# Optimization experiments

Measured on AMD Instinct MI355X. Metric: run time of the kernel, lower is better.

Reference implementation:

```python
import jax, jax.numpy as jnp
import numpy as np

N_NODES = 100000
N_EDGES = 6400000
IN_NODE = 6
IN_EDGE = 1
HID = 10
OUT = 2


def setup_inputs() -> dict:
    key = jax.random.key(0)
    ks = jax.random.split(key, 8)
    x = jax.random.normal(ks[0], (N_NODES, IN_NODE), dtype=jnp.float32)
    edge_index = jax.random.randint(ks[1], (2, N_EDGES), 0, N_NODES, dtype=jnp.int64)
    edge_attr = jax.random.normal(ks[2], (N_EDGES, IN_EDGE), dtype=jnp.float32)
    edge_attr_T = jax.random.normal(ks[3], (N_EDGES, IN_EDGE), dtype=jnp.float32)
    in_dim = 2 * IN_NODE + IN_EDGE  # 13
    W1 = jax.random.normal(ks[4], (in_dim, HID), dtype=jnp.float32) / np.sqrt(in_dim)
    b1 = jnp.zeros((HID,), dtype=jnp.float32)
    W2 = jax.random.normal(ks[5], (HID, OUT), dtype=jnp.float32) / np.sqrt(HID)
    b2 = jnp.zeros((OUT,), dtype=jnp.float32)
    return {"x": x, "edge_index": edge_index, "edge_attr": edge_attr,
            "edge_attr_T": edge_attr_T, "W1": W1, "b1": b1, "W2": W2, "b2": b2}


def _mlp(feat, W1, b1, W2, b2):
    h = jax.nn.relu(feat @ W1 + b1)
    return h @ W2 + b2


def reference(x, edge_index, edge_attr, edge_attr_T, W1, b1, W2, b2):
    src = edge_index[0]
    tgt = edge_index[1]
    x_src = x[src]  # [E, 6]
    x_tgt = x[tgt]  # [E, 6]
    feat_fwd = jnp.concatenate([x_src, x_tgt, edge_attr], axis=-1)      # [E, 13]
    feat_rev = jnp.concatenate([x_tgt, x_src, edge_attr_T], axis=-1)    # [E, 13]
    out = _mlp(feat_fwd, W1, b1, W2, b2) + _mlp(feat_rev, W1, b1, W2, b2)
    out = out * 0.5
    out = jax.nn.softmax(out, axis=1)
    return out[:, -1:]  # [E, 1]
```

## Files before the change

### kernel.cpp

```cpp
#include <hip/hip_runtime.h>
#include <hip/hip_fp16.h>


__global__ void prep(const float* __restrict__ W1, const float* __restrict__ b1,
                     const float* __restrict__ W2, const float* __restrict__ b2,
                     const float* __restrict__ x, float* __restrict__ ws, int N) {
    int t = blockIdx.x * 256 + threadIdx.x;
    if (t < N) {
        const float2* xr = (const float2*)x;
        float2 a0 = xr[3 * t], a1 = xr[3 * t + 1], a2 = xr[3 * t + 2];
        union { __half2 h[4]; float4 f; } pk;
        pk.h[0] = __floats2half2_rn(a0.x, a0.y);
        pk.h[1] = __floats2half2_rn(a1.x, a1.y);
        pk.h[2] = __floats2half2_rn(a2.x, a2.y);
        pk.h[3] = __floats2half2_rn(0.0f, 0.0f);
        ((float4*)((char*)ws + 4096))[t] = pk.f;
    }
    if (blockIdx.x == 0) {
        int u = threadIdx.x;
        if (u < 60) {
            int i = u / 10, j = u % 10;
            float a = W1[i * 10 + j];
            float c = W1[(i + 6) * 10 + j];
            ws[u]      = 0.5f * (a + c);
            ws[60 + u] = 0.5f * (a - c);
        }
        if (u < 10) {
            ws[120 + u] = W1[120 + u];
            ws[130 + u] = b1[u];
            ws[140 + u] = 0.5f * (W2[u * 2 + 1] - W2[u * 2]);
        }
        if (u == 0) ws[150] = b2[1] - b2[0];
    }
}

__launch_bounds__(256, 8)
__global__ void edge_mlp(const float4* __restrict__ xp, const int* __restrict__ ei,
                         const float* __restrict__ ea, const float* __restrict__ eaT,
                         const float* __restrict__ wg, float* __restrict__ out, int E) {
    int e = blockIdx.x * 256 + threadIdx.x;
    if (e >= E) return;

    int   si   = __builtin_nontemporal_load(ei + e);
    int   ti   = __builtin_nontemporal_load(ei + E + e);
    float fea  = __builtin_nontemporal_load(ea + e);
    float feaT = __builtin_nontemporal_load(eaT + e);

    float4 rs = xp[si];
    float4 rt = xp[ti];
    const __half2* hs = (const __half2*)&rs;
    const __half2* ht = (const __half2*)&rt;

    float sv[6], dv[6];
#pragma unroll
    for (int k = 0; k < 3; ++k) {
        float2 fs = __half22float2(hs[k]);
        float2 ft = __half22float2(ht[k]);
        sv[2 * k]     = fs.x + ft.x;  dv[2 * k]     = fs.x - ft.x;
        sv[2 * k + 1] = fs.y + ft.y;  dv[2 * k + 1] = fs.y - ft.y;
    }

    float cacc[10], macc[10];
#pragma unroll
    for (int j = 0; j < 10; ++j) { cacc[j] = wg[130 + j]; macc[j] = 0.0f; }
#pragma unroll
    for (int i = 0; i < 6; ++i) {
#pragma unroll
        for (int j = 0; j < 10; ++j) {
            cacc[j] = fmaf(sv[i], wg[i * 10 + j],      cacc[j]);
            macc[j] = fmaf(dv[i], wg[60 + i * 10 + j], macc[j]);
        }
    }

    float z = wg[150];
#pragma unroll
    for (int j = 0; j < 10; ++j) {
        float af = fmaf(fea,  wg[120 + j], cacc[j] + macc[j]);
        float ar = fmaf(feaT, wg[120 + j], cacc[j] - macc[j]);
        float h  = fmaxf(af, 0.0f) + fmaxf(ar, 0.0f);
        z = fmaf(h, wg[140 + j], z);
    }

    float r = 1.0f / (1.0f + __expf(-z));
    __builtin_nontemporal_store(r, out + e);
}

extern "C" void kernel_launch(void* const* d_in, const int* in_sizes, int n_in,
                              void* d_out, int out_size, void* d_ws, size_t ws_size,
                              hipStream_t stream) {
    const float* x   = (const float*)d_in[0];
    const int*   ei  = (const int*)d_in[1];
    const float* ea  = (const float*)d_in[2];
    const float* eaT = (const float*)d_in[3];
    const float* W1  = (const float*)d_in[4];
    const float* b1  = (const float*)d_in[5];
    const float* W2  = (const float*)d_in[6];
    const float* b2  = (const float*)d_in[7];
    float* out = (float*)d_out;
    float* ws  = (float*)d_ws;
    int E = in_sizes[2];
    int N = in_sizes[0] / 6;

    int pblocks = (N + 255) / 256;
    prep<<<pblocks, 256, 0, stream>>>(W1, b1, W2, b2, x, ws, N);

    const float4* xp = (const float4*)((char*)d_ws + 4096);
    int blocks = (E + 255) / 256;
    edge_mlp<<<blocks, 256, 0, stream>>>(xp, ei, ea, eaT, ws, out, E);
}
```

Baseline: 195.4 us.

## Use packed fp16 dot products and process two edges per thread

```diff
diff --git a/kernel.cpp b/kernel.cpp
--- a/kernel.cpp
+++ b/kernel.cpp
@@ -2,9 +2,16 @@
 #include <hip/hip_fp16.h>
 
 
+typedef _Float16 half2_t __attribute__((ext_vector_type(2)));
+typedef _Float16 half8_t __attribute__((ext_vector_type(8)));
+typedef float    float2_v __attribute__((ext_vector_type(2)));
+typedef int      int2_v   __attribute__((ext_vector_type(2)));
+
+union h2u { __half2 h; unsigned u; half2_t v; };
+
 __global__ void prep(const float* __restrict__ W1, const float* __restrict__ b1,
                      const float* __restrict__ W2, const float* __restrict__ b2,
-                     const float* __restrict__ x, float* __restrict__ ws, int N) {
+                     const float* __restrict__ x, float* __restrict__ wsf, int N) {
     int t = blockIdx.x * 256 + threadIdx.x;
     if (t < N) {
         const float2* xr = (const float2*)x;
@@ -14,75 +21,114 @@
         pk.h[1] = __floats2half2_rn(a1.x, a1.y);
         pk.h[2] = __floats2half2_rn(a2.x, a2.y);
         pk.h[3] = __floats2half2_rn(0.0f, 0.0f);
-        ((float4*)((char*)ws + 4096))[t] = pk.f;
+        ((float4*)((char*)wsf + 4096))[t] = pk.f;
     }
     if (blockIdx.x == 0) {
+        unsigned* wsu = (unsigned*)wsf;
         int u = threadIdx.x;
-        if (u < 60) {
-            int i = u / 10, j = u % 10;
-            float a = W1[i * 10 + j];
-            float c = W1[(i + 6) * 10 + j];
-            ws[u]      = 0.5f * (a + c);
-            ws[60 + u] = 0.5f * (a - c);
+        if (u < 10) wsf[u] = b1[u];
+        if (u == 0) wsf[10] = b2[1] - b2[0];
+        if (u < 30) {
+            int k = u / 10, j = u % 10;
+            float a0 = W1[(2 * k) * 10 + j],     c0 = W1[(2 * k + 6) * 10 + j];
+            float a1 = W1[(2 * k + 1) * 10 + j], c1 = W1[(2 * k + 7) * 10 + j];
+            h2u p, m;
+            p.h = __floats2half2_rn(0.5f * (a0 + c0), 0.5f * (a1 + c1));
+            m.h = __floats2half2_rn(0.5f * (a0 - c0), 0.5f * (a1 - c1));
+            wsu[16 + u] = p.u;
+            wsu[48 + u] = m.u;
         }
-        if (u < 10) {
-            ws[120 + u] = W1[120 + u];
-            ws[130 + u] = b1[u];
-            ws[140 + u] = 0.5f * (W2[u * 2 + 1] - W2[u * 2]);
+        if (u < 5) {
+            h2u a, b;
+            a.h = __floats2half2_rn(W1[120 + 2 * u], W1[120 + 2 * u + 1]);
+            b.h = __floats2half2_rn(0.5f * (W2[(2 * u) * 2 + 1] - W2[(2 * u) * 2]),
+                                    0.5f * (W2[(2 * u + 1) * 2 + 1] - W2[(2 * u + 1) * 2]));
+            wsu[80 + u] = a.u;
+            wsu[88 + u] = b.u;
         }
-        if (u == 0) ws[150] = b2[1] - b2[0];
     }
 }
 
-__launch_bounds__(256, 8)
-__global__ void edge_mlp(const float4* __restrict__ xp, const int* __restrict__ ei,
-                         const float* __restrict__ ea, const float* __restrict__ eaT,
-                         const float* __restrict__ wg, float* __restrict__ out, int E) {
-    int e = blockIdx.x * 256 + threadIdx.x;
-    if (e >= E) return;
+static __device__ __forceinline__ float fdot2(half2_t a, half2_t b, float c) {
+#if __has_builtin(__builtin_amdgcn_fdot2)
+    return __builtin_amdgcn_fdot2(a, b, c, false);
+#else
+    return fmaf((float)a[0], (float)b[0], fmaf((float)a[1], (float)b[1], c));
+#endif
+}
 
-    int   si   = __builtin_nontemporal_load(ei + e);
-    int   ti   = __builtin_nontemporal_load(ei + E + e);
-    float fea  = __builtin_nontemporal_load(ea + e);
-    float feaT = __builtin_nontemporal_load(eaT + e);
+static __device__ __forceinline__ half2_t h2bc(const unsigned* wsu, int idx) {
+    h2u t; t.u = wsu[idx]; return t.v;
+}
 
-    float4 rs = xp[si];
-    float4 rt = xp[ti];
-    const __half2* hs = (const __half2*)&rs;
-    const __half2* ht = (const __half2*)&rt;
-
-    float sv[6], dv[6];
-#pragma unroll
-    for (int k = 0; k < 3; ++k) {
-        float2 fs = __half22float2(hs[k]);
-        float2 ft = __half22float2(ht[k]);
-        sv[2 * k]     = fs.x + ft.x;  dv[2 * k]     = fs.x - ft.x;
-        sv[2 * k + 1] = fs.y + ft.y;  dv[2 * k + 1] = fs.y - ft.y;
-    }
+static __device__ __forceinline__ float edge_one(half8_t rs, half8_t rt,
+                                                 float fea, float feaT,
+                                                 const float* __restrict__ wsf,
+                                                 const unsigned* __restrict__ wsu) {
+    half8_t sv8 = rs + rt;
+    half8_t dv8 = rs - rt;
+    half2_t sv[3] = { __builtin_shufflevector(sv8, sv8, 0, 1),
+                      __builtin_shufflevector(sv8, sv8, 2, 3),
+                      __builtin_shufflevector(sv8, sv8, 4, 5) };
+    half2_t dv[3] = { __builtin_shufflevector(dv8, dv8, 0, 1),
+                      __builtin_shufflevector(dv8, dv8, 2, 3),
+                      __builtin_shufflevector(dv8, dv8, 4, 5) };
 
     float cacc[10], macc[10];
 #pragma unroll
-    for (int j = 0; j < 10; ++j) { cacc[j] = wg[130 + j]; macc[j] = 0.0f; }
+    for (int j = 0; j < 10; ++j) { cacc[j] = wsf[j]; macc[j] = 0.0f; }
 #pragma unroll
-    for (int i = 0; i < 6; ++i) {
+    for (int k = 0; k < 3; ++k) {
 #pragma unroll
         for (int j = 0; j < 10; ++j) {
-            cacc[j] = fmaf(sv[i], wg[i * 10 + j],      cacc[j]);
-            macc[j] = fmaf(dv[i], wg[60 + i * 10 + j], macc[j]);
+            cacc[j] = fdot2(sv[k], h2bc(wsu, 16 + k * 10 + j), cacc[j]);
+            macc[j] = fdot2(dv[k], h2bc(wsu, 48 + k * 10 + j), macc[j]);
         }
     }
 
-    float z = wg[150];
+    _Float16 feah  = (_Float16)fea,  feaTh = (_Float16)feaT;
+    half2_t fea2  = { feah,  feah  };
+    half2_t feaT2 = { feaTh, feaTh };
+    half2_t zero2 = { (_Float16)0.0f, (_Float16)0.0f };
+
+    float z = wsf[10];
 #pragma unroll
-    for (int j = 0; j < 10; ++j) {
-        float af = fmaf(fea,  wg[120 + j], cacc[j] + macc[j]);
-        float ar = fmaf(feaT, wg[120 + j], cacc[j] - macc[j]);
-        float h  = fmaxf(af, 0.0f) + fmaxf(ar, 0.0f);
-        z = fmaf(h, wg[140 + j], z);
+    for (int jp = 0; jp < 5; ++jp) {
+        half2_t c2 = { (_Float16)cacc[2 * jp], (_Float16)cacc[2 * jp + 1] };
+        half2_t m2 = { (_Float16)macc[2 * jp], (_Float16)macc[2 * jp + 1] };
+        half2_t w12 = h2bc(wsu, 80 + jp);
+        half2_t af2 = __builtin_elementwise_fma(fea2,  w12, c2 + m2);
+        half2_t ar2 = __builtin_elementwise_fma(feaT2, w12, c2 - m2);
+        half2_t h2  = __builtin_elementwise_max(af2, zero2) +
+                      __builtin_elementwise_max(ar2, zero2);
+        z = fdot2(h2, h2bc(wsu, 88 + jp), z);
     }
+    return 1.0f / (1.0f + __expf(-z));
+}
 
-    float r = 1.0f / (1.0f + __expf(-z));
-    __builtin_nontemporal_store(r, out + e);
+__launch_bounds__(256, 8)
+__global__ void edge_mlp(const half8_t* __restrict__ xp, const int* __restrict__ ei,
+                         const float* __restrict__ ea, const float* __restrict__ eaT,
+                         const float* __restrict__ wsf, float* __restrict__ out, int E) {
+    const unsigned* wsu = (const unsigned*)wsf;
+    int g = blockIdx.x * 256 + threadIdx.x;
+    int e0 = 2 * g;
+    if (e0 + 1 < E) {
+        int2_v   s2 = __builtin_nontemporal_load((const int2_v*)(ei + e0));
+        int2_v   t2 = __builtin_nontemporal_load((const int2_v*)(ei + E + e0));
+        float2_v fa = __builtin_nontemporal_load((const float2_v*)(ea + e0));
+        float2_v fT = __builtin_nontemporal_load((const float2_v*)(eaT + e0));
+        half8_t rs0 = xp[s2[0]], rt0 = xp[t2[0]];
+        half8_t rs1 = xp[s2[1]], rt1 = xp[t2[1]];
+        float2_v r;
+        r[0] = edge_one(rs0, rt0, fa[0], fT[0], wsf, wsu);
+        r[1] = edge_one(rs1, rt1, fa[1], fT[1], wsf, wsu);
+        __builtin_nontemporal_store(r, (float2_v*)(out + e0));
+    } else if (e0 < E) {
+        int si = ei[e0], ti = ei[E + e0];
+        float r = edge_one(xp[si], xp[ti], ea[e0], eaT[e0], wsf, wsu);
+        out[e0] = r;
+    }
 }
 
 extern "C" void kernel_launch(void* const* d_in, const int* in_sizes, int n_in,
@@ -104,7 +150,8 @@
     int pblocks = (N + 255) / 256;
     prep<<<pblocks, 256, 0, stream>>>(W1, b1, W2, b2, x, ws, N);
 
-    const float4* xp = (const float4*)((char*)d_ws + 4096);
-    int blocks = (E + 255) / 256;
+    const half8_t* xp = (const half8_t*)((char*)d_ws + 4096);
+    int nthreads = (E + 1) / 2;
+    int blocks = (nthreads + 255) / 256;
     edge_mlp<<<blocks, 256, 0, stream>>>(xp, ei, ea, eaT, ws, out, E);
 }
```

New measurement: 197.8 us. About the same (+1.2%).
